# Kernel optimization log

Measured on AMD Instinct MI355X. Metric: run time of the kernel, lower is better.

Reference implementation:

```python
import jax, jax.numpy as jnp
import numpy as np

V = 50000   # vocab_size
E = 300     # embed_dim (GRU input size)
H = 256     # hidden_dim
R = 2048    # number of replies
L0 = 128    # original content length
LR = 64     # max reply length (padded)

def setup_inputs() -> dict:
    key = jax.random.key(0)
    ks = jax.random.split(key, 20)
    s = 0.05
    inp = {
        "original_tokens": jax.random.randint(ks[0], (L0,), 0, V),
        "reply_tokens":    jax.random.randint(ks[1], (R, LR), 0, V),
        "reply_lengths":   jax.random.randint(ks[2], (R,), 1, LR + 1),
        "label":           jax.random.uniform(ks[3], (1,), dtype=jnp.float32),
        # learned params
        "embed": jax.random.normal(ks[4], (V, E), dtype=jnp.float32) * s,
        # bi-GRU forward direction (PyTorch layout: gates [r, z, n] stacked)
        "Wih_f": jax.random.normal(ks[5], (3 * H, E), dtype=jnp.float32) * s,
        "Whh_f": jax.random.normal(ks[6], (3 * H, H), dtype=jnp.float32) * s,
        "bih_f": jax.random.normal(ks[7], (3 * H,), dtype=jnp.float32) * s,
        "bhh_f": jax.random.normal(ks[8], (3 * H,), dtype=jnp.float32) * s,
        # bi-GRU reverse direction
        "Wih_b": jax.random.normal(ks[9], (3 * H, E), dtype=jnp.float32) * s,
        "Whh_b": jax.random.normal(ks[10], (3 * H, H), dtype=jnp.float32) * s,
        "bih_b": jax.random.normal(ks[11], (3 * H,), dtype=jnp.float32) * s,
        "bhh_b": jax.random.normal(ks[12], (3 * H,), dtype=jnp.float32) * s,
        # self.linear : 2H -> H
        "Wl": jax.random.normal(ks[13], (H, 2 * H), dtype=jnp.float32) * s,
        "bl": jax.random.normal(ks[14], (H,), dtype=jnp.float32) * s,
        # self.output_linear : H -> 1 (batch_size = 1)
        "Wo": jax.random.normal(ks[15], (1, H), dtype=jnp.float32) * s,
        "bo": jax.random.normal(ks[16], (1,), dtype=jnp.float32) * s,
    }
    return inp


def _gru_dir(x, Wih, Whh, bih, bhh):
    """Single-direction GRU over x: (S, E) -> (ys: (S, H), hT: (H,)).
    PyTorch gate math: r,z,n with n = tanh(gi_n + r * gh_n)."""
    def step(h, xt):
        gi = Wih @ xt + bih            # (3H,)
        gh = Whh @ h + bhh             # (3H,)
        r = jax.nn.sigmoid(gi[:H] + gh[:H])
        z = jax.nn.sigmoid(gi[H:2 * H] + gh[H:2 * H])
        n = jnp.tanh(gi[2 * H:] + r * gh[2 * H:])
        h_new = (1.0 - z) * n + z * h
        return h_new, h_new
    h0 = jnp.zeros((H,), dtype=x.dtype)
    hT, ys = jax.lax.scan(step, h0, x)
    return ys, hT


def reference(original_tokens, reply_tokens, reply_lengths, label,
              embed, Wih_f, Whh_f, bih_f, bhh_f,
              Wih_b, Whh_b, bih_b, bhh_b, Wl, bl, Wo, bo):
    # per-event embedding + sum pooling (batched replacement of Python loop)
    orig = embed[original_tokens].sum(axis=0)                      # (E,)
    mask = (jnp.arange(LR)[None, :] < reply_lengths[:, None]).astype(embed.dtype)
    rep = jnp.einsum('rle,rl->re', embed[reply_tokens], mask)      # (R, E)
    X = jnp.concatenate([orig[None, :], rep], axis=0)              # (S, E), S = R+1

    # bidirectional GRU (batch dim is 1, squeezed)
    ys_f, h_f = _gru_dir(X, Wih_f, Whh_f, bih_f, bhh_f)            # (S, H), (H,)
    ys_b, h_b = _gru_dir(X[::-1], Wih_b, Whh_b, bih_b, bhh_b)
    ys_b = ys_b[::-1]                                              # (S, H)

    out2 = jnp.concatenate([ys_f, ys_b], axis=-1)                  # (S, 2H)
    output = out2 @ Wl.T + bl                                      # (S, H)

    # hidden = sum over directions of final hidden states
    hsum = h_f + h_b                                               # (H,)

    # dot-product attention: query = hsum, keys = values = output
    scores = output @ hsum                                         # (S,)
    w = jax.nn.softmax(scores)                                     # attention dist
    ctx = w @ output                                               # (H,)

    result = jax.nn.sigmoid(ctx @ Wo.T + bo)                       # (1,)
    loss = (label - result) ** 2                                   # (1,)
    return (output[:, None, :], loss, result)                      # output: (S,1,H)
```

## Files before the change

kernel.cpp:

```cpp
#include <hip/hip_runtime.h>
#include <cstdint>
#include <cstddef>

#define NV 50000
#define NE 300
#define NH 256
#define NR 2048
#define NL0 128
#define NLR 64
#define NS 2049
#define G3 768
#define NWG 8
#define EPW 32

static constexpr size_t alignUp(size_t x, size_t a) { return (x + a - 1) / a * a; }
static constexpr size_t OFF_MAIL   = 0;
static constexpr size_t MAIL_U64S  = 2ull * 2 * NWG * NH;
static constexpr size_t OFF_CTX    = OFF_MAIL + MAIL_U64S * 8;
static constexpr size_t OFF_SCORES = OFF_CTX + 1024;
static constexpr size_t OFF_X      = alignUp(OFF_SCORES + (size_t)NS * 4, 256);
static constexpr size_t OFF_GI_F   = alignUp(OFF_X + (size_t)NS * NE * 4, 256);
static constexpr size_t OFF_GI_B   = alignUp(OFF_GI_F + (size_t)NS * G3 * 4, 256);
static constexpr size_t OFF_OUT2   = alignUp(OFF_GI_B + (size_t)NS * G3 * 4, 256);

__global__ __launch_bounds__(320) void embed_sum_kernel(
    const int* __restrict__ otok, const int* __restrict__ rtok,
    const int* __restrict__ rlen, const float* __restrict__ embed,
    float* __restrict__ X)
{
    const int b = blockIdx.x;
    const int e = threadIdx.x;
    if (e >= NE) return;
    float acc = 0.f;
    if (b == 0) {
        for (int t = 0; t < NL0; ++t) {
            int tok = otok[t];
            acc += embed[(size_t)tok * NE + e];
        }
    } else {
        const int r = b - 1;
        const int L = rlen[r];
        const int* tr = rtok + (size_t)r * NLR;
        for (int t = 0; t < L; ++t) {
            int tok = tr[t];
            acc += embed[(size_t)tok * NE + e];
        }
    }
    X[(size_t)b * NE + e] = acc;
}

__global__ __launch_bounds__(256) void gemm_abt(
    const float* __restrict__ A, const float* __restrict__ B,
    const float* __restrict__ bias, float* __restrict__ C,
    int M, int N, int K, int ldc)
{
    __shared__ float As[16][65];
    __shared__ float Bs[16][65];
    const int bm = blockIdx.x * 64, bn = blockIdx.y * 64;
    const int tid = threadIdx.x;
    const int tx = tid & 15, ty = tid >> 4;
    float acc[4][4] = {};
    for (int k0 = 0; k0 < K; k0 += 16) {
        #pragma unroll
        for (int i = 0; i < 4; ++i) {
            int l = tid + 256 * i;
            int mm = l >> 4, kk = l & 15;
            int gm = bm + mm, gk = k0 + kk;
            As[kk][mm] = (gm < M && gk < K) ? A[(size_t)gm * K + gk] : 0.f;
            int gn = bn + mm;
            Bs[kk][mm] = (gk < K) ? B[(size_t)gn * K + gk] : 0.f;
        }
        __syncthreads();
        #pragma unroll
        for (int kk = 0; kk < 16; ++kk) {
            float a0 = As[kk][ty], a1 = As[kk][ty+16], a2 = As[kk][ty+32], a3 = As[kk][ty+48];
            float b0 = Bs[kk][tx], b1 = Bs[kk][tx+16], b2 = Bs[kk][tx+32], b3 = Bs[kk][tx+48];
            acc[0][0] += a0*b0; acc[0][1] += a0*b1; acc[0][2] += a0*b2; acc[0][3] += a0*b3;
            acc[1][0] += a1*b0; acc[1][1] += a1*b1; acc[1][2] += a1*b2; acc[1][3] += a1*b3;
            acc[2][0] += a2*b0; acc[2][1] += a2*b1; acc[2][2] += a2*b2; acc[2][3] += a2*b3;
            acc[3][0] += a3*b0; acc[3][1] += a3*b1; acc[3][2] += a3*b2; acc[3][3] += a3*b3;
        }
        __syncthreads();
    }
    #pragma unroll
    for (int i = 0; i < 4; ++i) {
        int gm = bm + ty + 16 * i;
        if (gm >= M) continue;
        #pragma unroll
        for (int j = 0; j < 4; ++j) {
            int gn = bn + tx + 16 * j;
            C[(size_t)gm * ldc + gn] = acc[i][j] + bias[gn];
        }
    }
}

__global__ __launch_bounds__(512) void gru_kernel(
    const float* __restrict__ Whh_f, const float* __restrict__ bhh_f,
    const float* __restrict__ Whh_b, const float* __restrict__ bhh_b,
    const float* __restrict__ gi_f, const float* __restrict__ gi_b,
    float* __restrict__ out2,
    unsigned long long* __restrict__ mail)
{
    const int dir = blockIdx.x >> 3;
    const int w   = blockIdx.x & 7;
    const int tid = threadIdx.x;

    const float* __restrict__ Whh = dir ? Whh_b : Whh_f;
    const float* __restrict__ bhh = dir ? bhh_b : bhh_f;
    const float* __restrict__ gi  = dir ? gi_b  : gi_f;
    unsigned long long* __restrict__ mbase = mail + (size_t)dir * (2 * NWG * NH);

    __shared__ __align__(16) float hbuf[2][NH];

    if (tid < NH) hbuf[0][tid] = 0.f;

    float4 wr[8], wz[8], wn[8];
    float bhr = 0.f, bhz = 0.f, bhn = 0.f;
    float gir = 0.f, giz = 0.f, gin = 0.f;
    int e = 0, j = 0;

    if (tid < 256) {
        e = w * EPW + (tid >> 3);
        j = tid & 7;
        const float* r0 = Whh + (size_t)e * NH;
        const float* r1 = Whh + (size_t)(NH + e) * NH;
        const float* r2 = Whh + (size_t)(2 * NH + e) * NH;
        #pragma unroll
        for (int c = 0; c < 8; ++c) {
            int off = c * 32 + j * 4;
            wr[c] = *(const float4*)(r0 + off);
            wz[c] = *(const float4*)(r1 + off);
            wn[c] = *(const float4*)(r2 + off);
        }
        bhr = bhh[e]; bhz = bhh[NH + e]; bhn = bhh[2 * NH + e];
        const float* g0 = gi + (size_t)(dir ? NS - 1 : 0) * G3 + e;
        gir = g0[0]; giz = g0[NH]; gin = g0[2 * NH];
    }
    __syncthreads();

    for (int t = 0; t < NS; ++t) {
        const int p = t & 1;
        if (tid < 256) {
            const int s = dir ? (NS - 1 - t) : t;
            float girN = 0.f, gizN = 0.f, ginN = 0.f;
            if (t < NS - 1) {
                const float* gn = gi + (size_t)(dir ? (NS - 2 - t) : (t + 1)) * G3 + e;
                girN = gn[0]; gizN = gn[NH]; ginN = gn[2 * NH];
            }
            const float hprev = hbuf[p][e];
            const float4* hq = (const float4*)hbuf[p];
            float ar = 0.f, az = 0.f, an = 0.f;
            #pragma unroll
            for (int c = 0; c < 8; ++c) {
                float4 h4 = hq[c * 8 + j];
                ar += wr[c].x*h4.x + wr[c].y*h4.y + wr[c].z*h4.z + wr[c].w*h4.w;
                az += wz[c].x*h4.x + wz[c].y*h4.y + wz[c].z*h4.z + wz[c].w*h4.w;
                an += wn[c].x*h4.x + wn[c].y*h4.y + wn[c].z*h4.z + wn[c].w*h4.w;
            }
            ar += __shfl_xor(ar, 1); az += __shfl_xor(az, 1); an += __shfl_xor(an, 1);
            ar += __shfl_xor(ar, 2); az += __shfl_xor(az, 2); an += __shfl_xor(an, 2);
            ar += __shfl_xor(ar, 4); az += __shfl_xor(az, 4); an += __shfl_xor(an, 4);
            const float r  = 1.f / (1.f + __expf(-(gir + ar + bhr)));
            const float z  = 1.f / (1.f + __expf(-(giz + az + bhz)));
            const float n  = tanhf(gin + r * (an + bhn));
            const float hn = (1.f - z) * n + z * hprev;
            if (t < NS - 1) {
                if (j != w) {
                    unsigned long long pv =
                        ((unsigned long long)(unsigned)(t + 1) << 32) |
                        (unsigned long long)__float_as_uint(hn);
                    __hip_atomic_store(&mbase[((size_t)p * NWG + j) * NH + e], pv,
                                       __ATOMIC_RELAXED, __HIP_MEMORY_SCOPE_AGENT);
                }
                if (j == 0) hbuf[p ^ 1][e] = hn;
            }
            if (j == 0) out2[(size_t)s * (2 * NH) + dir * NH + e] = hn;
            gir = girN; giz = gizN; gin = ginN;
        } else {
            const int slot = tid - 256;
            if (t < NS - 1 && (slot >> 5) != w) {
                const unsigned want = (unsigned)(t + 1);
                unsigned long long v;
                do {
                    v = __hip_atomic_load(&mbase[((size_t)p * NWG + w) * NH + slot],
                                          __ATOMIC_RELAXED, __HIP_MEMORY_SCOPE_AGENT);
                } while ((unsigned)(v >> 32) != want);
                hbuf[p ^ 1][slot] = __uint_as_float((unsigned)v);
            }
        }
        asm volatile("s_waitcnt lgkmcnt(0)\n\ts_barrier" ::: "memory");
    }
}

__global__ __launch_bounds__(256) void scores_kernel(
    const float* __restrict__ outp, const float* __restrict__ out2,
    float* __restrict__ scores)
{
    const int s = blockIdx.x, m = threadIdx.x;
    float hs = out2[(size_t)(NS - 1) * (2 * NH) + m] + out2[NH + m];
    float v = outp[(size_t)s * NH + m] * hs;
    #pragma unroll
    for (int o = 32; o > 0; o >>= 1) v += __shfl_down(v, o);
    __shared__ float p[4];
    if ((m & 63) == 0) p[m >> 6] = v;
    __syncthreads();
    if (m == 0) scores[s] = p[0] + p[1] + p[2] + p[3];
}

__global__ __launch_bounds__(1024) void softmax_kernel(float* __restrict__ sc)
{
    const int tid = threadIdx.x;
    __shared__ float red[16];
    float x0 = (tid < NS) ? sc[tid] : -3.0e38f;
    float x1 = (tid + 1024 < NS) ? sc[tid + 1024] : -3.0e38f;
    float mx = fmaxf(x0, x1);
    #pragma unroll
    for (int o = 32; o > 0; o >>= 1) mx = fmaxf(mx, __shfl_xor(mx, o));
    if ((tid & 63) == 0) red[tid >> 6] = mx;
    __syncthreads();
    if (tid == 0) {
        float m = red[0];
        for (int i = 1; i < 16; ++i) m = fmaxf(m, red[i]);
        red[0] = m;
    }
    __syncthreads();
    const float gmax = red[0];
    float e0 = (tid < NS) ? __expf(x0 - gmax) : 0.f;
    float e1 = (tid + 1024 < NS) ? __expf(x1 - gmax) : 0.f;
    float sm = e0 + e1;
    #pragma unroll
    for (int o = 32; o > 0; o >>= 1) sm += __shfl_xor(sm, o);
    __syncthreads();
    if ((tid & 63) == 0) red[tid >> 6] = sm;
    __syncthreads();
    if (tid == 0) {
        float su = 0.f;
        for (int i = 0; i < 16; ++i) su += red[i];
        red[1] = 1.f / su;
    }
    __syncthreads();
    const float inv = red[1];
    if (tid < NS) sc[tid] = e0 * inv;
    if (tid + 1024 < NS) sc[tid + 1024] = e1 * inv;
}

__global__ __launch_bounds__(256) void ctx_kernel(
    const float* __restrict__ outp, const float* __restrict__ w,
    float* __restrict__ ctx)
{
    const int m = threadIdx.x;
    const int s0 = blockIdx.x * 128;
    const int s1 = min(s0 + 128, NS);
    float acc = 0.f;
    for (int s = s0; s < s1; ++s) acc += w[s] * outp[(size_t)s * NH + m];
    atomicAdd(&ctx[m], acc);
}

__global__ __launch_bounds__(256) void final_kernel(
    const float* __restrict__ ctx, const float* __restrict__ Wo,
    const float* __restrict__ bo, const float* __restrict__ label,
    float* __restrict__ dout)
{
    const int m = threadIdx.x;
    float v = ctx[m] * Wo[m];
    #pragma unroll
    for (int o = 32; o > 0; o >>= 1) v += __shfl_down(v, o);
    __shared__ float p[4];
    if ((m & 63) == 0) p[m >> 6] = v;
    __syncthreads();
    if (m == 0) {
        float x = p[0] + p[1] + p[2] + p[3] + bo[0];
        float result = 1.f / (1.f + __expf(-x));
        float d = label[0] - result;
        dout[(size_t)NS * NH]     = d * d;
        dout[(size_t)NS * NH + 1] = result;
    }
}

extern "C" void kernel_launch(void* const* d_in, const int* in_sizes, int n_in,
                              void* d_out, int out_size, void* d_ws, size_t ws_size,
                              hipStream_t stream)
{
    const int*   otok  = (const int*)d_in[0];
    const int*   rtok  = (const int*)d_in[1];
    const int*   rlen  = (const int*)d_in[2];
    const float* label = (const float*)d_in[3];
    const float* embed = (const float*)d_in[4];
    const float* Wih_f = (const float*)d_in[5];
    const float* Whh_f = (const float*)d_in[6];
    const float* bih_f = (const float*)d_in[7];
    const float* bhh_f = (const float*)d_in[8];
    const float* Wih_b = (const float*)d_in[9];
    const float* Whh_b = (const float*)d_in[10];
    const float* bih_b = (const float*)d_in[11];
    const float* bhh_b = (const float*)d_in[12];
    const float* Wl    = (const float*)d_in[13];
    const float* bl    = (const float*)d_in[14];
    const float* Wo    = (const float*)d_in[15];
    const float* bo    = (const float*)d_in[16];

    char* ws = (char*)d_ws;
    unsigned long long* mail = (unsigned long long*)(ws + OFF_MAIL);
    float* ctx    = (float*)(ws + OFF_CTX);
    float* scores = (float*)(ws + OFF_SCORES);
    float* X      = (float*)(ws + OFF_X);
    float* gi_f   = (float*)(ws + OFF_GI_F);
    float* gi_b   = (float*)(ws + OFF_GI_B);
    float* out2   = (float*)(ws + OFF_OUT2);
    float* outp   = (float*)d_out;

    hipMemsetAsync(d_ws, 0, OFF_SCORES, stream);

    embed_sum_kernel<<<NS, 320, 0, stream>>>(otok, rtok, rlen, embed, X);

    gemm_abt<<<dim3(33, 12), 256, 0, stream>>>(X, Wih_f, bih_f, gi_f, NS, G3, NE, G3);
    gemm_abt<<<dim3(33, 12), 256, 0, stream>>>(X, Wih_b, bih_b, gi_b, NS, G3, NE, G3);

    gru_kernel<<<16, 512, 0, stream>>>(Whh_f, bhh_f, Whh_b, bhh_b,
                                       gi_f, gi_b, out2, mail);

    gemm_abt<<<dim3(33, 4), 256, 0, stream>>>(out2, Wl, bl, outp, NS, NH, 2 * NH, NH);

    scores_kernel<<<NS, 256, 0, stream>>>(outp, out2, scores);
    softmax_kernel<<<1, 1024, 0, stream>>>(scores);
    ctx_kernel<<<(NS + 127) / 128, 256, 0, stream>>>(outp, scores, ctx);
    final_kernel<<<1, 256, 0, stream>>>(ctx, Wo, bo, label, (float*)d_out);
}
```

Measured before the change: 3.395 ms.

## Run each GRU direction in one workgroup with fp16 register-resident weights

Replaces the 8-workgroup-per-direction recurrence and its global-memory mailbox handshake with a single 512-thread workgroup per direction. Each thread pair owns one hidden unit and keeps its half of the three Whh rows in registers as packed fp16, computing the dot products with fdot2 and combining the halves through a DPP add. Per-step synchronisation becomes a plain workgroup barrier instead of polling atomics across CUs. The cost is lower precision from fp16 weights and hidden state in the matvec, plus heavy register pressure from 192 half2 registers per thread, which risks spills.

```diff
diff --git a/kernel.cpp b/kernel.cpp
--- a/kernel.cpp
+++ b/kernel.cpp
@@ -10,18 +10,26 @@
 #define NLR 64
 #define NS 2049
 #define G3 768
-#define NWG 8
-#define EPW 32
 
 static constexpr size_t alignUp(size_t x, size_t a) { return (x + a - 1) / a * a; }
-static constexpr size_t OFF_MAIL   = 0;
-static constexpr size_t MAIL_U64S  = 2ull * 2 * NWG * NH;
-static constexpr size_t OFF_CTX    = OFF_MAIL + MAIL_U64S * 8;
+static constexpr size_t OFF_CTX    = 0;
 static constexpr size_t OFF_SCORES = OFF_CTX + 1024;
 static constexpr size_t OFF_X      = alignUp(OFF_SCORES + (size_t)NS * 4, 256);
 static constexpr size_t OFF_GI_F   = alignUp(OFF_X + (size_t)NS * NE * 4, 256);
 static constexpr size_t OFF_GI_B   = alignUp(OFF_GI_F + (size_t)NS * G3 * 4, 256);
 static constexpr size_t OFF_OUT2   = alignUp(OFF_GI_B + (size_t)NS * G3 * 4, 256);
+
+typedef _Float16 half2t __attribute__((ext_vector_type(2)));
+
+#if __has_builtin(__builtin_amdgcn_fdot2)
+__device__ __forceinline__ float fdot2(half2t a, half2t b, float c) {
+    return __builtin_amdgcn_fdot2(a, b, c, false);
+}
+#else
+__device__ __forceinline__ float fdot2(half2t a, half2t b, float c) {
+    return c + (float)a[0] * (float)b[0] + (float)a[1] * (float)b[1];
+}
+#endif
 
 __global__ __launch_bounds__(320) void embed_sum_kernel(
     const int* __restrict__ otok, const int* __restrict__ rtok,
@@ -94,45 +102,48 @@
     }
 }
 
+__device__ __forceinline__ float dpp_add_xor1(float x) {
+    int v = __builtin_amdgcn_update_dpp(0, __float_as_int(x), 0xB1, 0xF, 0xF, true);
+    return x + __int_as_float(v);
+}
+
 __global__ __launch_bounds__(512) void gru_kernel(
     const float* __restrict__ Whh_f, const float* __restrict__ bhh_f,
     const float* __restrict__ Whh_b, const float* __restrict__ bhh_b,
     const float* __restrict__ gi_f, const float* __restrict__ gi_b,
-    float* __restrict__ out2,
-    unsigned long long* __restrict__ mail)
-{
-    const int dir = blockIdx.x >> 3;
-    const int w   = blockIdx.x & 7;
-    const int tid = threadIdx.x;
+    float* __restrict__ out2)
+{
+    const int dir  = blockIdx.x;
+    const int tid  = threadIdx.x;
+    const int e    = tid >> 1;
+    const int hsel = tid & 1;
 
     const float* __restrict__ Whh = dir ? Whh_b : Whh_f;
     const float* __restrict__ bhh = dir ? bhh_b : bhh_f;
     const float* __restrict__ gi  = dir ? gi_b  : gi_f;
-    unsigned long long* __restrict__ mbase = mail + (size_t)dir * (2 * NWG * NH);
-
-    __shared__ __align__(16) float hbuf[2][NH];
-
-    if (tid < NH) hbuf[0][tid] = 0.f;
-
-    float4 wr[8], wz[8], wn[8];
-    float bhr = 0.f, bhz = 0.f, bhn = 0.f;
-    float gir = 0.f, giz = 0.f, gin = 0.f;
-    int e = 0, j = 0;
-
-    if (tid < 256) {
-        e = w * EPW + (tid >> 3);
-        j = tid & 7;
-        const float* r0 = Whh + (size_t)e * NH;
-        const float* r1 = Whh + (size_t)(NH + e) * NH;
-        const float* r2 = Whh + (size_t)(2 * NH + e) * NH;
-        #pragma unroll
-        for (int c = 0; c < 8; ++c) {
-            int off = c * 32 + j * 4;
-            wr[c] = *(const float4*)(r0 + off);
-            wz[c] = *(const float4*)(r1 + off);
-            wn[c] = *(const float4*)(r2 + off);
-        }
-        bhr = bhh[e]; bhz = bhh[NH + e]; bhn = bhh[2 * NH + e];
+
+    __shared__ __align__(16) _Float16 hl16[2][NH];
+    __shared__ float hf32[2][NH];
+
+    if (tid < NH) { hl16[0][tid] = (_Float16)0.f; hf32[0][tid] = 0.f; }
+
+    half2t wr[64], wz[64], wn[64];
+    {
+        const float2* r0 = (const float2*)(Whh + (size_t)e * NH            + hsel * 128);
+        const float2* r1 = (const float2*)(Whh + (size_t)(NH + e) * NH     + hsel * 128);
+        const float2* r2 = (const float2*)(Whh + (size_t)(2 * NH + e) * NH + hsel * 128);
+        #pragma unroll
+        for (int c = 0; c < 64; ++c) {
+            float2 a = r0[c], b = r1[c], d = r2[c];
+            wr[c] = half2t{(_Float16)a.x, (_Float16)a.y};
+            wz[c] = half2t{(_Float16)b.x, (_Float16)b.y};
+            wn[c] = half2t{(_Float16)d.x, (_Float16)d.y};
+        }
+    }
+    const float bhr = bhh[e], bhz = bhh[NH + e], bhn = bhh[2 * NH + e];
+
+    float gir, giz, gin;
+    {
         const float* g0 = gi + (size_t)(dir ? NS - 1 : 0) * G3 + e;
         gir = g0[0]; giz = g0[NH]; gin = g0[2 * NH];
     }
@@ -140,55 +151,47 @@
 
     for (int t = 0; t < NS; ++t) {
         const int p = t & 1;
-        if (tid < 256) {
-            const int s = dir ? (NS - 1 - t) : t;
-            float girN = 0.f, gizN = 0.f, ginN = 0.f;
-            if (t < NS - 1) {
-                const float* gn = gi + (size_t)(dir ? (NS - 2 - t) : (t + 1)) * G3 + e;
-                girN = gn[0]; gizN = gn[NH]; ginN = gn[2 * NH];
-            }
-            const float hprev = hbuf[p][e];
-            const float4* hq = (const float4*)hbuf[p];
-            float ar = 0.f, az = 0.f, an = 0.f;
-            #pragma unroll
-            for (int c = 0; c < 8; ++c) {
-                float4 h4 = hq[c * 8 + j];
-                ar += wr[c].x*h4.x + wr[c].y*h4.y + wr[c].z*h4.z + wr[c].w*h4.w;
-                az += wz[c].x*h4.x + wz[c].y*h4.y + wz[c].z*h4.z + wz[c].w*h4.w;
-                an += wn[c].x*h4.x + wn[c].y*h4.y + wn[c].z*h4.z + wn[c].w*h4.w;
-            }
-            ar += __shfl_xor(ar, 1); az += __shfl_xor(az, 1); an += __shfl_xor(an, 1);
-            ar += __shfl_xor(ar, 2); az += __shfl_xor(az, 2); an += __shfl_xor(an, 2);
-            ar += __shfl_xor(ar, 4); az += __shfl_xor(az, 4); an += __shfl_xor(an, 4);
-            const float r  = 1.f / (1.f + __expf(-(gir + ar + bhr)));
-            const float z  = 1.f / (1.f + __expf(-(giz + az + bhz)));
-            const float n  = tanhf(gin + r * (an + bhn));
-            const float hn = (1.f - z) * n + z * hprev;
-            if (t < NS - 1) {
-                if (j != w) {
-                    unsigned long long pv =
-                        ((unsigned long long)(unsigned)(t + 1) << 32) |
-                        (unsigned long long)__float_as_uint(hn);
-                    __hip_atomic_store(&mbase[((size_t)p * NWG + j) * NH + e], pv,
-                                       __ATOMIC_RELAXED, __HIP_MEMORY_SCOPE_AGENT);
-                }
-                if (j == 0) hbuf[p ^ 1][e] = hn;
-            }
-            if (j == 0) out2[(size_t)s * (2 * NH) + dir * NH + e] = hn;
-            gir = girN; giz = gizN; gin = ginN;
-        } else {
-            const int slot = tid - 256;
-            if (t < NS - 1 && (slot >> 5) != w) {
-                const unsigned want = (unsigned)(t + 1);
-                unsigned long long v;
-                do {
-                    v = __hip_atomic_load(&mbase[((size_t)p * NWG + w) * NH + slot],
-                                          __ATOMIC_RELAXED, __HIP_MEMORY_SCOPE_AGENT);
-                } while ((unsigned)(v >> 32) != want);
-                hbuf[p ^ 1][slot] = __uint_as_float((unsigned)v);
-            }
-        }
-        asm volatile("s_waitcnt lgkmcnt(0)\n\ts_barrier" ::: "memory");
+        const int s = dir ? (NS - 1 - t) : t;
+
+        float girN = 0.f, gizN = 0.f, ginN = 0.f;
+        if (t < NS - 1) {
+            const float* gn = gi + (size_t)(dir ? (NS - 2 - t) : (t + 1)) * G3 + e;
+            girN = gn[0]; gizN = gn[NH]; ginN = gn[2 * NH];
+        }
+
+        const float hprev = hf32[p][e];
+        const uint4* hq = (const uint4*)&hl16[p][hsel * 128];
+
+        float ar0 = 0.f, ar1 = 0.f, az0 = 0.f, az1 = 0.f, an0 = 0.f, an1 = 0.f;
+        #pragma unroll
+        for (int c = 0; c < 16; ++c) {
+            uint4 q = hq[c];
+            half2t h0 = __builtin_bit_cast(half2t, q.x);
+            half2t h1 = __builtin_bit_cast(half2t, q.y);
+            half2t h2 = __builtin_bit_cast(half2t, q.z);
+            half2t h3 = __builtin_bit_cast(half2t, q.w);
+            ar0 = fdot2(wr[c*4+0], h0, ar0); az0 = fdot2(wz[c*4+0], h0, az0); an0 = fdot2(wn[c*4+0], h0, an0);
+            ar1 = fdot2(wr[c*4+1], h1, ar1); az1 = fdot2(wz[c*4+1], h1, az1); an1 = fdot2(wn[c*4+1], h1, an1);
+            ar0 = fdot2(wr[c*4+2], h2, ar0); az0 = fdot2(wz[c*4+2], h2, az0); an0 = fdot2(wn[c*4+2], h2, an0);
+            ar1 = fdot2(wr[c*4+3], h3, ar1); az1 = fdot2(wz[c*4+3], h3, az1); an1 = fdot2(wn[c*4+3], h3, an1);
+        }
+        float ar = ar0 + ar1, az = az0 + az1, an = an0 + an1;
+        ar = dpp_add_xor1(ar);
+        az = dpp_add_xor1(az);
+        an = dpp_add_xor1(an);
+
+        const float r  = 1.f / (1.f + __expf(-(gir + ar + bhr)));
+        const float z  = 1.f / (1.f + __expf(-(giz + az + bhz)));
+        const float n  = tanhf(gin + r * (an + bhn));
+        const float hn = (1.f - z) * n + z * hprev;
+
+        if (hsel == 0) {
+            hf32[p ^ 1][e] = hn;
+            hl16[p ^ 1][e] = (_Float16)hn;
+            out2[(size_t)s * (2 * NH) + dir * NH + e] = hn;
+        }
+        gir = girN; giz = gizN; gin = ginN;
+        __syncthreads();
     }
 }
 
@@ -300,7 +303,6 @@
     const float* bo    = (const float*)d_in[16];
 
     char* ws = (char*)d_ws;
-    unsigned long long* mail = (unsigned long long*)(ws + OFF_MAIL);
     float* ctx    = (float*)(ws + OFF_CTX);
     float* scores = (float*)(ws + OFF_SCORES);
     float* X      = (float*)(ws + OFF_X);
@@ -309,15 +311,15 @@
     float* out2   = (float*)(ws + OFF_OUT2);
     float* outp   = (float*)d_out;
 
-    hipMemsetAsync(d_ws, 0, OFF_SCORES, stream);
+    hipMemsetAsync(ws + OFF_CTX, 0, 1024, stream);
 
     embed_sum_kernel<<<NS, 320, 0, stream>>>(otok, rtok, rlen, embed, X);
 
     gemm_abt<<<dim3(33, 12), 256, 0, stream>>>(X, Wih_f, bih_f, gi_f, NS, G3, NE, G3);
     gemm_abt<<<dim3(33, 12), 256, 0, stream>>>(X, Wih_b, bih_b, gi_b, NS, G3, NE, G3);
 
-    gru_kernel<<<16, 512, 0, stream>>>(Whh_f, bhh_f, Whh_b, bhh_b,
-                                       gi_f, gi_b, out2, mail);
+    gru_kernel<<<2, 512, 0, stream>>>(Whh_f, bhh_f, Whh_b, bhh_b,
+                                      gi_f, gi_b, out2);
 
     gemm_abt<<<dim3(33, 4), 256, 0, stream>>>(out2, Wl, bl, outp, NS, NH, 2 * NH, NH);
 
```

Measured after the change: 2.867 ms. 1.18x faster.
